# Optimization experiments

Measured on AMD Instinct MI355X. Metric: run time of the kernel, lower is better.

The kernel has to match this reference:

```python
import jax, jax.numpy as jnp
import numpy as np

B, L, D_MODEL, N_HEADS = 2, 2048, 2048, 16
HEAD_DIM = D_MODEL // N_HEADS
EPS = 1e-6
ROPE_THETA = 10000.0


def rms_norm(x, scale):
    # normalize over head_dim, learnable per-dim scale (QKNorm)
    var = jnp.mean(jnp.square(x), axis=-1, keepdims=True)
    return x * jax.lax.rsqrt(var + EPS) * scale


def rope(x, offset=0):
    # x: [B, H, T, D]; rotate-half rotary embedding over flattened positions
    T, D = x.shape[-2], x.shape[-1]
    half = D // 2
    inv_freq = 1.0 / (ROPE_THETA ** (jnp.arange(0, half, dtype=jnp.float32) / half))
    pos = jnp.arange(T, dtype=jnp.float32) + offset
    ang = pos[:, None] * inv_freq[None, :]            # [T, half]
    cos, sin = jnp.cos(ang), jnp.sin(ang)
    x1, x2 = x[..., :half], x[..., half:]
    return jnp.concatenate([x1 * cos - x2 * sin, x1 * sin + x2 * cos], axis=-1)


def setup_inputs() -> dict:
    key = jax.random.key(0)
    ks = jax.random.split(key, 7)
    s = 1.0 / np.sqrt(D_MODEL)
    x = jax.random.normal(ks[0], (B, L, D_MODEL), dtype=jnp.float32)
    w_qkv = jax.random.uniform(ks[1], (D_MODEL, 3 * D_MODEL), jnp.float32, -s, s)
    b_qkv = jax.random.uniform(ks[2], (3 * D_MODEL,), jnp.float32, -s, s)
    q_scale = jnp.ones((HEAD_DIM,), jnp.float32)
    k_scale = jnp.ones((HEAD_DIM,), jnp.float32)
    w_out = jax.random.uniform(ks[3], (D_MODEL, D_MODEL), jnp.float32, -s, s)
    b_out = jax.random.uniform(ks[4], (D_MODEL,), jnp.float32, -s, s)
    mask = jnp.tril(jnp.ones((L, L), dtype=bool))   # causal block mask pattern
    return {"x": x, "w_qkv": w_qkv, "b_qkv": b_qkv, "q_scale": q_scale,
            "k_scale": k_scale, "w_out": w_out, "b_out": b_out, "mask": mask}


def reference(x, w_qkv, b_qkv, q_scale, k_scale, w_out, b_out, mask):
    b, t, _ = x.shape
    qkv = x @ w_qkv + b_qkv                                   # [B, T, 3*D]
    qkv = qkv.reshape(b, t, 3, N_HEADS, HEAD_DIM)
    q, k, v = jnp.moveaxis(qkv, 2, 0)                          # each [B, T, H, D]
    q = jnp.transpose(q, (0, 2, 1, 3))                         # [B, H, T, D]
    k = jnp.transpose(k, (0, 2, 1, 3))
    v = jnp.transpose(v, (0, 2, 1, 3))
    q = rms_norm(q, q_scale)
    k = rms_norm(k, k_scale)
    q = rope(q, offset=0)
    k = rope(k, offset=0)
    scores = jnp.einsum('bhqd,bhkd->bhqk', q, k) / np.sqrt(HEAD_DIM)
    scores = jnp.where(mask[None, None, :, :], scores, jnp.float32(-1e30))
    attn = jax.nn.softmax(scores, axis=-1)
    out = jnp.einsum('bhqk,bhkd->bhqd', attn, v)               # [B, H, T, D]
    out = jnp.transpose(out, (0, 2, 1, 3)).reshape(b, t, D_MODEL)
    return out @ w_out + b_out
```

## Files before the change

kernel.cpp:

```cpp
#include <hip/hip_runtime.h>
#include <hip/hip_bf16.h>
#include <stdint.h>


typedef unsigned short ushort8 __attribute__((ext_vector_type(8)));
typedef short          bf16x8 __attribute__((ext_vector_type(8)));
typedef float          f32x4  __attribute__((ext_vector_type(4)));

#define B_   2
#define L_   2048
#define DM   2048
#define NH   16
#define HD   128
#define QKVW 6144

__device__ __forceinline__ uint16_t f2bf(float f){
  uint32_t u = __builtin_bit_cast(uint32_t, f);
  u += 0x7FFFu + ((u >> 16) & 1u);
  return (uint16_t)(u >> 16);
}
__device__ __forceinline__ float bf2f(uint16_t h){
  uint32_t u = ((uint32_t)h) << 16;
  return __builtin_bit_cast(float, u);
}

#define GLD16(gp, lp) __builtin_amdgcn_global_load_lds( \
  (const __attribute__((address_space(1))) void*)(gp),  \
  (__attribute__((address_space(3))) void*)(lp), 16, 0, 0)

__global__ __launch_bounds__(256) void rope_table(float* __restrict__ ct, float* __restrict__ st){
  int i = blockIdx.x * 256 + threadIdx.x;
  int t = i >> 6, d = i & 63;
  float invf = powf(10000.f, -(float)d * (1.f/64.f));
  float s, c;
  sincosf((float)t * invf, &s, &c);
  ct[i] = c; st[i] = s;
}

__global__ __launch_bounds__(256) void cvt_f32_bf16(const float* __restrict__ x,
                                                    uint16_t* __restrict__ o, int n8){
  int i = blockIdx.x * 256 + threadIdx.x;
  if (i < n8){
    const float4* xv = (const float4*)x;
    float4 a = xv[(size_t)i*2], b = xv[(size_t)i*2+1];
    ushort8 v;
    v[0]=f2bf(a.x); v[1]=f2bf(a.y); v[2]=f2bf(a.z); v[3]=f2bf(a.w);
    v[4]=f2bf(b.x); v[5]=f2bf(b.y); v[6]=f2bf(b.z); v[7]=f2bf(b.w);
    *(ushort8*)(o + (size_t)i*8) = v;
  }
}

__global__ __launch_bounds__(256) void transpose_w(const float* __restrict__ W,
                                                   uint16_t* __restrict__ Wt, int R, int C){
  __shared__ float T[64][65];
  const int rb = blockIdx.x, cb = blockIdx.y;
  const int tid = threadIdx.x;
#pragma unroll
  for (int i=0;i<4;i++){
    int rr = i*16 + (tid >> 4);
    int cc = (tid & 15) * 4;
    float4 v = *(const float4*)(W + (size_t)(rb*64 + rr) * C + cb*64 + cc);
    T[rr][cc] = v.x; T[rr][cc+1] = v.y; T[rr][cc+2] = v.z; T[rr][cc+3] = v.w;
  }
  __syncthreads();
  const int oc = tid >> 2, rc = (tid & 3) * 16;
  ushort8 o0, o1;
#pragma unroll
  for (int j=0;j<8;j++){ o0[j] = f2bf(T[rc+j][oc]); o1[j] = f2bf(T[rc+8+j][oc]); }
  size_t ob = (size_t)(cb*64 + oc) * R + rb*64 + rc;
  *(ushort8*)(Wt + ob)     = o0;
  *(ushort8*)(Wt + ob + 8) = o1;
}

template<int OUTB>
__global__ __launch_bounds__(512, 2) void gemm8p(
    const uint16_t* __restrict__ A, const uint16_t* __restrict__ Bt,
    const float* __restrict__ bias, void* __restrict__ Cv,
    int M, int N, int K, int nbn)
{
  __shared__ uint16_t LA[3*16384];
  __shared__ uint16_t LB[3*8192];
  const int nwg = (M >> 8) * nbn;
  const int q8  = nwg >> 3;
  const int id  = ((int)blockIdx.x & 7) * q8 + ((int)blockIdx.x >> 3);
  const int bm = id / nbn, bn = id % nbn;
  const int tid = threadIdx.x;
  const int lane = tid & 63, w = tid >> 6;
  const int wm = w & 3, wn = w >> 2;
  const int l15 = lane & 15, lh = lane >> 4;
  const int NT = K >> 6;

  const int qs3 = ((lane & 7) ^ ((lane >> 3) & 7)) * 8;
  const uint16_t* gA_ = A  + (size_t)((bm << 8) + (w << 5) + (lane >> 3)) * K + qs3;
  const uint16_t* gB_ = Bt + (size_t)((bn << 7) + (w << 4) + (lane >> 3)) * K + qs3;
  uint16_t* lA_ = LA + (w << 11);
  uint16_t* lB_ = LB + (w << 10);

  const int sw0 = ((lh       ^ (l15 & 7)) << 3);
  const int sw1 = (((4 | lh) ^ (l15 & 7)) << 3);
  const int aoff = (((wm << 6) + l15) << 6);
  const int boff = (((wn << 6) + l15) << 6);

  f32x4 acc[4][4];
#pragma unroll
  for (int i=0;i<4;i++)
#pragma unroll
    for (int j=0;j<4;j++) acc[i][j] = f32x4{0.f,0.f,0.f,0.f};

  auto STAGE_A = [&](int tt, int s, int i){
    GLD16(gA_ + (size_t)tt*64 + (size_t)(i*8)*K, lA_ + s*16384 + i*512);
  };
  auto STAGE_B = [&](int tt, int s, int i){
    GLD16(gB_ + (size_t)tt*64 + (size_t)(i*8)*K, lB_ + s*8192 + i*512);
  };

#pragma unroll
  for (int i=0;i<4;i++) STAGE_A(0, 0, i);
#pragma unroll
  for (int i=0;i<2;i++) STAGE_B(0, 0, i);
#pragma unroll
  for (int i=0;i<4;i++) STAGE_A(1, 1, i);
#pragma unroll
  for (int i=0;i<2;i++) STAGE_B(1, 1, i);
  asm volatile("s_waitcnt vmcnt(6)" ::: "memory");
  __builtin_amdgcn_s_barrier();

  int sl = 0, sl2 = 2;
  for (int t = 0; t < NT; ++t){
    const bool pf = (t + 2 < NT);
    const uint16_t* la = LA + sl*16384;
    const uint16_t* lb = LB + sl*8192;

    bf16x8 af0[4], bf0[4], af1[4], bf1[4];
#pragma unroll
    for (int mi=0;mi<4;mi++) af0[mi] = *(const bf16x8*)(la + aoff + mi*1024 + sw0);
#pragma unroll
    for (int ni=0;ni<4;ni++) bf0[ni] = *(const bf16x8*)(lb + boff + ni*1024 + sw0);
#pragma unroll
    for (int mi=0;mi<4;mi++) af1[mi] = *(const bf16x8*)(la + aoff + mi*1024 + sw1);
#pragma unroll
    for (int ni=0;ni<4;ni++) bf1[ni] = *(const bf16x8*)(lb + boff + ni*1024 + sw1);
    if (pf){
      STAGE_A(t+2, sl2, 0); STAGE_A(t+2, sl2, 1);
      STAGE_A(t+2, sl2, 2); STAGE_A(t+2, sl2, 3);
      STAGE_B(t+2, sl2, 0); STAGE_B(t+2, sl2, 1);
    }
    __builtin_amdgcn_s_setprio(1);
#pragma unroll
    for (int mi=0;mi<4;mi++)
#pragma unroll
      for (int ni=0;ni<4;ni++)
        acc[mi][ni] = __builtin_amdgcn_mfma_f32_16x16x32_bf16(af0[mi], bf0[ni], acc[mi][ni], 0, 0, 0);
#pragma unroll
    for (int mi=0;mi<4;mi++)
#pragma unroll
      for (int ni=0;ni<4;ni++)
        acc[mi][ni] = __builtin_amdgcn_mfma_f32_16x16x32_bf16(af1[mi], bf1[ni], acc[mi][ni], 0, 0, 0);
    __builtin_amdgcn_s_setprio(0);

    if (t < NT-2)       { asm volatile("s_waitcnt vmcnt(6)" ::: "memory"); }
    else if (t == NT-2) { asm volatile("s_waitcnt vmcnt(0)" ::: "memory"); }
    if (t < NT-1) __builtin_amdgcn_s_barrier();
    sl  = (sl  == 2) ? 0 : sl  + 1;
    sl2 = (sl2 == 2) ? 0 : sl2 + 1;
  }

  const int cm = (bm << 8) + (wm << 6);
  const int cn = (bn << 7) + (wn << 6);
#pragma unroll
  for (int ni=0;ni<4;ni++){
    int col = cn + ni*16 + l15;
    float bs = bias[col];
#pragma unroll
    for (int mi=0;mi<4;mi++){
#pragma unroll
      for (int r=0;r<4;r++){
        int rowg = cm + mi*16 + lh*4 + r;
        float v = acc[mi][ni][r] + bs;
        if (OUTB) ((uint16_t*)Cv)[(size_t)rowg * N + col] = f2bf(v);
        else      ((float*)Cv)[(size_t)rowg * N + col] = v;
      }
    }
  }
}

__global__ __launch_bounds__(256) void rmsrope(
    uint16_t* __restrict__ qkv, const float* __restrict__ qs, const float* __restrict__ ks,
    const float* __restrict__ ct, const float* __restrict__ st)
{
  const int bx  = blockIdx.x;
  const int t   = bx & (L_-1);
  const int tid = threadIdx.x;
  const int h   = tid >> 4;
  const int dq  = (tid & 15) * 8;
  const int dd  = dq & 63;
  const bool hi = dq >= 64;
  const size_t base = (size_t)bx * QKVW;
  float cs[8], sn[8];
#pragma unroll
  for (int j=0;j<8;j++){ cs[j] = ct[(size_t)t*64 + dd + j]; sn[j] = st[(size_t)t*64 + dd + j]; }
#pragma unroll
  for (int qk = 0; qk < 2; qk++){
    uint16_t* p = qkv + base + qk*DM + h*HD + dq;
    ushort8 vv = *(const ushort8*)p;
    float x[8]; float ssum = 0.f;
#pragma unroll
    for (int j=0;j<8;j++){ x[j] = bf2f(vv[j]); ssum += x[j]*x[j]; }
    ssum += __shfl_xor(ssum, 1); ssum += __shfl_xor(ssum, 2);
    ssum += __shfl_xor(ssum, 4); ssum += __shfl_xor(ssum, 8);
    const float inv = rsqrtf(ssum * (1.f/128.f) + 1e-6f);
    const float* sc = qk ? ks : qs;
    float y[8];
#pragma unroll
    for (int j=0;j<8;j++) y[j] = x[j] * inv * sc[dq + j];
    float z[8];
#pragma unroll
    for (int j=0;j<8;j++) z[j] = __shfl_xor(y[j], 8);
    ushort8 o;
#pragma unroll
    for (int j=0;j<8;j++){
      float r = hi ? (z[j]*sn[j] + y[j]*cs[j])
                   : (y[j]*cs[j] - z[j]*sn[j]);
      o[j] = f2bf(r);
    }
    *(ushort8*)p = o;
  }
}

__global__ __launch_bounds__(256) void transpose_v(const uint16_t* __restrict__ qkv,
                                                   uint16_t* __restrict__ vt){
  __shared__ uint16_t T[64][136];
  const int tb = blockIdx.x, bh = blockIdx.y;
  const int b = bh >> 4, h = bh & 15;
  const int tid = threadIdx.x;
#pragma unroll
  for (int i=0;i<4;i++){
    int g = i*256 + tid, tt = g >> 4, c = g & 15;
    *(ushort8*)(&T[tt][c*8]) =
      *(const ushort8*)(qkv + ((size_t)b*L_ + tb*64 + tt)*QKVW + 2*DM + h*HD + c*8);
  }
  __syncthreads();
  const int d = tid >> 1, th = tid & 1;
#pragma unroll
  for (int i=0;i<4;i++){
    ushort8 o;
#pragma unroll
    for (int j=0;j<8;j++) o[j] = T[th*32 + i*8 + j][d];
    *(ushort8*)(vt + ((size_t)bh*HD + d)*L_ + tb*64 + th*32 + i*8) = o;
  }
}

__global__ __launch_bounds__(256) void flash_attn(
    const uint16_t* __restrict__ qkv, const uint16_t* __restrict__ vt,
    uint16_t* __restrict__ ao)
{
  const int qp = blockIdx.x;
  const int bh = blockIdx.y;
  const int b = bh >> 4, h = bh & 15;
  const int tid = threadIdx.x;
  const int lane = tid & 63, w = tid >> 6;
  const int l15 = lane & 15, lh = lane >> 4;

  __shared__ uint16_t Ks[64][136];
  __shared__ uint16_t Vs[128][72];
  __shared__ uint16_t Ps[4][16][72];

  const float SCL = 0.12751744f;

  for (int sel = 0; sel < 2; sel++){
    const int qb = sel ? (31 - qp) : qp;

    const size_t qrow = (size_t)b * L_ + qb*64 + w*16 + l15;
    const uint16_t* qp_ = qkv + qrow * QKVW + h * HD;
    bf16x8 qf[4];
#pragma unroll
    for (int c = 0; c < 4; c++) qf[c] = *(const bf16x8*)(qp_ + c*32 + lh*8);

    float m_s = -3.0e38f, l_s = 0.f;
    f32x4 oacc[8];
#pragma unroll
    for (int nt = 0; nt < 8; nt++) oacc[nt] = f32x4{0.f,0.f,0.f,0.f};

    const int ntile = qb + 1;
    ushort8 rk[4], rv[4];

#pragma unroll
    for (int i = 0; i < 4; i++){
      int g = i*256 + tid, row = g >> 4, c = g & 15;
      rk[i] = *(const ushort8*)(qkv + ((size_t)b*L_ + row)*QKVW + DM + h*HD + c*8);
    }
#pragma unroll
    for (int i = 0; i < 4; i++){
      int g = i*256 + tid, d = g >> 3, c = g & 7;
      rv[i] = *(const ushort8*)(vt + ((size_t)bh*HD + d)*L_ + c*8);
    }

    for (int kt = 0; kt < ntile; kt++){
      __syncthreads();
#pragma unroll
      for (int i = 0; i < 4; i++){ int g = i*256+tid; *(ushort8*)(&Ks[g>>4][(g&15)*8]) = rk[i]; }
#pragma unroll
      for (int i = 0; i < 4; i++){ int g = i*256+tid; *(ushort8*)(&Vs[g>>3][(g&7)*8]) = rv[i]; }
      __syncthreads();

      if (kt + 1 < ntile){
        const int k2 = (kt + 1) * 64;
#pragma unroll
        for (int i = 0; i < 4; i++){
          int g = i*256 + tid, row = g >> 4, c = g & 15;
          rk[i] = *(const ushort8*)(qkv + ((size_t)b*L_ + k2 + row)*QKVW + DM + h*HD + c*8);
        }
#pragma unroll
        for (int i = 0; i < 4; i++){
          int g = i*256 + tid, d = g >> 3, c = g & 7;
          rv[i] = *(const ushort8*)(vt + ((size_t)bh*HD + d)*L_ + k2 + c*8);
        }
      }

      f32x4 s[4];
#pragma unroll
      for (int nt = 0; nt < 4; nt++) s[nt] = f32x4{0.f,0.f,0.f,0.f};
      __builtin_amdgcn_s_setprio(1);
#pragma unroll
      for (int c = 0; c < 4; c++){
#pragma unroll
        for (int nt = 0; nt < 4; nt++){
          bf16x8 kf = *(const bf16x8*)(&Ks[nt*16 + l15][c*32 + lh*8]);
          s[nt] = __builtin_amdgcn_mfma_f32_16x16x32_bf16(kf, qf[c], s[nt], 0, 0, 0);
        }
      }
      __builtin_amdgcn_s_setprio(0);

      const bool diag = (kt == qb);
      const int qg = w*16 + l15;
      const int kb = lh*4;
#pragma unroll
      for (int nt = 0; nt < 4; nt++){
#pragma unroll
        for (int r = 0; r < 4; r++){
          float v = s[nt][r] * SCL;
          if (diag && (nt*16 + kb + r > qg)) v = -1.0e30f;
          s[nt][r] = v;
        }
      }
      float pm = s[0][0];
#pragma unroll
      for (int nt = 0; nt < 4; nt++)
#pragma unroll
        for (int r = 0; r < 4; r++) pm = fmaxf(pm, s[nt][r]);
      pm = fmaxf(pm, __shfl_xor(pm, 16));
      pm = fmaxf(pm, __shfl_xor(pm, 32));
      if (!__all(pm - m_s <= 8.0f)){
        float mn = fmaxf(m_s, pm);
        float alpha = exp2f(m_s - mn);
        m_s = mn; l_s *= alpha;
        float ar[4];
#pragma unroll
        for (int r = 0; r < 4; r++) ar[r] = __shfl(alpha, lh*4 + r);
#pragma unroll
        for (int nt = 0; nt < 8; nt++)
#pragma unroll
          for (int r = 0; r < 4; r++) oacc[nt][r] *= ar[r];
      }
      float rs = 0.f;
#pragma unroll
      for (int nt = 0; nt < 4; nt++){
        float p0 = exp2f(s[nt][0] - m_s);
        float p1 = exp2f(s[nt][1] - m_s);
        float p2 = exp2f(s[nt][2] - m_s);
        float p3 = exp2f(s[nt][3] - m_s);
        rs += (p0 + p1) + (p2 + p3);
        uint2 pk;
        pk.x = (uint32_t)f2bf(p0) | ((uint32_t)f2bf(p1) << 16);
        pk.y = (uint32_t)f2bf(p2) | ((uint32_t)f2bf(p3) << 16);
        *(uint2*)(&Ps[w][l15][nt*16 + kb]) = pk;
      }
      rs += __shfl_xor(rs, 16);
      rs += __shfl_xor(rs, 32);
      l_s += rs;

      asm volatile("s_waitcnt lgkmcnt(0)" ::: "memory");
      __builtin_amdgcn_s_setprio(1);
#pragma unroll
      for (int kc = 0; kc < 2; kc++){
        bf16x8 pf = *(const bf16x8*)(&Ps[w][l15][kc*32 + lh*8]);
#pragma unroll
        for (int nt = 0; nt < 8; nt++){
          bf16x8 vf = *(const bf16x8*)(&Vs[nt*16 + l15][kc*32 + lh*8]);
          oacc[nt] = __builtin_amdgcn_mfma_f32_16x16x32_bf16(pf, vf, oacc[nt], 0, 0, 0);
        }
      }
      __builtin_amdgcn_s_setprio(0);
    }
    float invl[4];
#pragma unroll
    for (int r = 0; r < 4; r++) invl[r] = 1.f / __shfl(l_s, lh*4 + r);
#pragma unroll
    for (int nt = 0; nt < 8; nt++){
#pragma unroll
      for (int r = 0; r < 4; r++){
        float v = oacc[nt][r] * invl[r];
        size_t row = (size_t)b*L_ + qb*64 + w*16 + lh*4 + r;
        ao[row * DM + h*HD + nt*16 + l15] = f2bf(v);
      }
    }
  }
}

extern "C" void kernel_launch(void* const* d_in, const int* in_sizes, int n_in,
                              void* d_out, int out_size, void* d_ws, size_t ws_size,
                              hipStream_t stream)
{
  (void)in_sizes; (void)n_in; (void)out_size; (void)ws_size;
  const float* x       = (const float*)d_in[0];
  const float* w_qkv   = (const float*)d_in[1];
  const float* b_qkv   = (const float*)d_in[2];
  const float* q_scale = (const float*)d_in[3];
  const float* k_scale = (const float*)d_in[4];
  const float* w_out   = (const float*)d_in[5];
  const float* b_out   = (const float*)d_in[6];
  float* out = (float*)d_out;

  char* ws = (char*)d_ws;
  uint16_t* qkv   = (uint16_t*)(ws);
  uint16_t* reg1  = (uint16_t*)(ws + 50331648);
  uint16_t* reg2  = (uint16_t*)(ws + 50331648 + 16777216);
  uint16_t* woutT = (uint16_t*)(ws + 50331648 + 16777216 + 25165824);
  float*    ct    = (float*)(ws + 100663296);
  float*    st    = ct + 131072;

  uint16_t* xb    = reg1;
  uint16_t* ao    = reg1;
  uint16_t* wqkvT = reg2;
  uint16_t* vt    = reg2;

  rope_table  <<<512, 256, 0, stream>>>(ct, st);
  cvt_f32_bf16<<<4096, 256, 0, stream>>>(x, xb, 1048576);
  transpose_w <<<dim3(32, 96), 256, 0, stream>>>(w_qkv, wqkvT, 2048, 6144);
  transpose_w <<<dim3(32, 32), 256, 0, stream>>>(w_out, woutT, 2048, 2048);
  gemm8p<1>   <<<768, 512, 0, stream>>>(xb, wqkvT, b_qkv, qkv, 4096, 6144, 2048, 48);
  rmsrope     <<<4096, 256, 0, stream>>>(qkv, q_scale, k_scale, ct, st);
  transpose_v <<<dim3(32, 32), 256, 0, stream>>>(qkv, vt);
  flash_attn  <<<dim3(16, 32), 256, 0, stream>>>(qkv, vt, ao);
  gemm8p<0>   <<<256, 512, 0, stream>>>(ao, woutT, b_out, out, 4096, 2048, 2048, 16);
}
```

Measured before the change: 281.5 us.

## Double query rows per flash-attention block with XOR-swizzled shared memory

Each wave in the flash attention kernel now handles 32 query rows, two 16-row tiles, instead of 16. The query block grows from 64 to 128, so every loaded K/V tile feeds twice as many MFMAs and global K/V traffic is halved. The shared-memory tiles drop their padding and use XOR swizzling to avoid bank conflicts, and the grid is reordered to put batch-head in x. The cost is fewer blocks (256 instead of 512), more registers per thread, and extra masked compute on the two diagonal tiles.

```diff
diff --git a/kernel.cpp b/kernel.cpp
--- a/kernel.cpp
+++ b/kernel.cpp
@@ -254,34 +254,39 @@
     const uint16_t* __restrict__ qkv, const uint16_t* __restrict__ vt,
     uint16_t* __restrict__ ao)
 {
-  const int qp = blockIdx.x;
-  const int bh = blockIdx.y;
+  const int bh = blockIdx.x;
+  const int qp = blockIdx.y;
   const int b = bh >> 4, h = bh & 15;
   const int tid = threadIdx.x;
   const int lane = tid & 63, w = tid >> 6;
   const int l15 = lane & 15, lh = lane >> 4;
-
-  __shared__ uint16_t Ks[64][136];
-  __shared__ uint16_t Vs[128][72];
-  __shared__ uint16_t Ps[4][16][72];
+  const int e3 = l15 & 7;
+
+  __shared__ uint16_t Ks[64][128];
+  __shared__ uint16_t Vs[128][64];
+  __shared__ uint16_t Ps[4][32][64];
 
   const float SCL = 0.12751744f;
 
   for (int sel = 0; sel < 2; sel++){
-    const int qb = sel ? (31 - qp) : qp;
-
-    const size_t qrow = (size_t)b * L_ + qb*64 + w*16 + l15;
-    const uint16_t* qp_ = qkv + qrow * QKVW + h * HD;
-    bf16x8 qf[4];
-#pragma unroll
-    for (int c = 0; c < 4; c++) qf[c] = *(const bf16x8*)(qp_ + c*32 + lh*8);
-
-    float m_s = -3.0e38f, l_s = 0.f;
-    f32x4 oacc[8];
-#pragma unroll
-    for (int nt = 0; nt < 8; nt++) oacc[nt] = f32x4{0.f,0.f,0.f,0.f};
-
-    const int ntile = qb + 1;
+    const int Q = sel ? (15 - qp) : qp;
+
+    const size_t qbase = (size_t)b * L_ + Q*128 + w*32;
+    bf16x8 qf[2][4];
+#pragma unroll
+    for (int qt = 0; qt < 2; qt++)
+#pragma unroll
+      for (int c = 0; c < 4; c++)
+        qf[qt][c] = *(const bf16x8*)(qkv + (qbase + qt*16 + l15)*QKVW + h*HD + c*32 + lh*8);
+
+    float m_s[2] = {-3.0e38f, -3.0e38f}, l_s[2] = {0.f, 0.f};
+    f32x4 oacc[2][8];
+#pragma unroll
+    for (int qt = 0; qt < 2; qt++)
+#pragma unroll
+      for (int nt = 0; nt < 8; nt++) oacc[qt][nt] = f32x4{0.f,0.f,0.f,0.f};
+
+    const int ntile = 2*Q + 2;
     ushort8 rk[4], rv[4];
 
 #pragma unroll
@@ -298,9 +303,15 @@
     for (int kt = 0; kt < ntile; kt++){
       __syncthreads();
 #pragma unroll
-      for (int i = 0; i < 4; i++){ int g = i*256+tid; *(ushort8*)(&Ks[g>>4][(g&15)*8]) = rk[i]; }
-#pragma unroll
-      for (int i = 0; i < 4; i++){ int g = i*256+tid; *(ushort8*)(&Vs[g>>3][(g&7)*8]) = rv[i]; }
+      for (int i = 0; i < 4; i++){
+        int g = i*256 + tid, row = g >> 4, c = g & 15;
+        *(ushort8*)(&Ks[row][(c ^ (row & 7))*8]) = rk[i];
+      }
+#pragma unroll
+      for (int i = 0; i < 4; i++){
+        int g = i*256 + tid, d = g >> 3, c = g & 7;
+        *(ushort8*)(&Vs[d][(c ^ (d & 7))*8]) = rv[i];
+      }
       __syncthreads();
 
       if (kt + 1 < ntile){
@@ -317,91 +328,117 @@
         }
       }
 
-      f32x4 s[4];
-#pragma unroll
-      for (int nt = 0; nt < 4; nt++) s[nt] = f32x4{0.f,0.f,0.f,0.f};
+      f32x4 s[2][4];
+#pragma unroll
+      for (int qt = 0; qt < 2; qt++)
+#pragma unroll
+        for (int nt = 0; nt < 4; nt++) s[qt][nt] = f32x4{0.f,0.f,0.f,0.f};
       __builtin_amdgcn_s_setprio(1);
 #pragma unroll
       for (int c = 0; c < 4; c++){
 #pragma unroll
         for (int nt = 0; nt < 4; nt++){
-          bf16x8 kf = *(const bf16x8*)(&Ks[nt*16 + l15][c*32 + lh*8]);
-          s[nt] = __builtin_amdgcn_mfma_f32_16x16x32_bf16(kf, qf[c], s[nt], 0, 0, 0);
+          bf16x8 kf = *(const bf16x8*)(&Ks[nt*16 + l15][(((c<<2)|lh) ^ e3)*8]);
+          s[0][nt] = __builtin_amdgcn_mfma_f32_16x16x32_bf16(kf, qf[0][c], s[0][nt], 0, 0, 0);
+          s[1][nt] = __builtin_amdgcn_mfma_f32_16x16x32_bf16(kf, qf[1][c], s[1][nt], 0, 0, 0);
         }
       }
       __builtin_amdgcn_s_setprio(0);
 
-      const bool diag = (kt == qb);
-      const int qg = w*16 + l15;
+      const bool edge = (kt >= 2*Q);
       const int kb = lh*4;
-#pragma unroll
-      for (int nt = 0; nt < 4; nt++){
-#pragma unroll
-        for (int r = 0; r < 4; r++){
-          float v = s[nt][r] * SCL;
-          if (diag && (nt*16 + kb + r > qg)) v = -1.0e30f;
-          s[nt][r] = v;
-        }
-      }
-      float pm = s[0][0];
-#pragma unroll
-      for (int nt = 0; nt < 4; nt++)
-#pragma unroll
-        for (int r = 0; r < 4; r++) pm = fmaxf(pm, s[nt][r]);
-      pm = fmaxf(pm, __shfl_xor(pm, 16));
-      pm = fmaxf(pm, __shfl_xor(pm, 32));
-      if (!__all(pm - m_s <= 8.0f)){
-        float mn = fmaxf(m_s, pm);
-        float alpha = exp2f(m_s - mn);
-        m_s = mn; l_s *= alpha;
-        float ar[4];
-#pragma unroll
-        for (int r = 0; r < 4; r++) ar[r] = __shfl(alpha, lh*4 + r);
-#pragma unroll
-        for (int nt = 0; nt < 8; nt++)
-#pragma unroll
-          for (int r = 0; r < 4; r++) oacc[nt][r] *= ar[r];
-      }
-      float rs = 0.f;
-#pragma unroll
-      for (int nt = 0; nt < 4; nt++){
-        float p0 = exp2f(s[nt][0] - m_s);
-        float p1 = exp2f(s[nt][1] - m_s);
-        float p2 = exp2f(s[nt][2] - m_s);
-        float p3 = exp2f(s[nt][3] - m_s);
-        rs += (p0 + p1) + (p2 + p3);
-        uint2 pk;
-        pk.x = (uint32_t)f2bf(p0) | ((uint32_t)f2bf(p1) << 16);
-        pk.y = (uint32_t)f2bf(p2) | ((uint32_t)f2bf(p3) << 16);
-        *(uint2*)(&Ps[w][l15][nt*16 + kb]) = pk;
-      }
-      rs += __shfl_xor(rs, 16);
-      rs += __shfl_xor(rs, 32);
-      l_s += rs;
+      const int q0 = Q*128 + w*32 + l15;
+      const int kglob0 = kt*64 + kb;
+#pragma unroll
+      for (int qt = 0; qt < 2; qt++){
+        const int qg = q0 + qt*16;
+#pragma unroll
+        for (int nt = 0; nt < 4; nt++){
+#pragma unroll
+          for (int r = 0; r < 4; r++){
+            float v = s[qt][nt][r] * SCL;
+            if (edge && (kglob0 + nt*16 + r > qg)) v = -1.0e30f;
+            s[qt][nt][r] = v;
+          }
+        }
+      }
+      float pm[2];
+#pragma unroll
+      for (int qt = 0; qt < 2; qt++){
+        float v = s[qt][0][0];
+#pragma unroll
+        for (int nt = 0; nt < 4; nt++)
+#pragma unroll
+          for (int r = 0; r < 4; r++) v = fmaxf(v, s[qt][nt][r]);
+        v = fmaxf(v, __shfl_xor(v, 16));
+        v = fmaxf(v, __shfl_xor(v, 32));
+        pm[qt] = v;
+      }
+      float grow = fmaxf(pm[0] - m_s[0], pm[1] - m_s[1]);
+      if (!__all(grow <= 8.0f)){
+#pragma unroll
+        for (int qt = 0; qt < 2; qt++){
+          float mn = fmaxf(m_s[qt], pm[qt]);
+          float alpha = exp2f(m_s[qt] - mn);
+          m_s[qt] = mn; l_s[qt] *= alpha;
+          float ar[4];
+#pragma unroll
+          for (int r = 0; r < 4; r++) ar[r] = __shfl(alpha, lh*4 + r);
+#pragma unroll
+          for (int nt = 0; nt < 8; nt++)
+#pragma unroll
+            for (int r = 0; r < 4; r++) oacc[qt][nt][r] *= ar[r];
+        }
+      }
+#pragma unroll
+      for (int qt = 0; qt < 2; qt++){
+        float rs = 0.f;
+#pragma unroll
+        for (int nt = 0; nt < 4; nt++){
+          float p0 = exp2f(s[qt][nt][0] - m_s[qt]);
+          float p1 = exp2f(s[qt][nt][1] - m_s[qt]);
+          float p2 = exp2f(s[qt][nt][2] - m_s[qt]);
+          float p3 = exp2f(s[qt][nt][3] - m_s[qt]);
+          rs += (p0 + p1) + (p2 + p3);
+          uint2 pk;
+          pk.x = (uint32_t)f2bf(p0) | ((uint32_t)f2bf(p1) << 16);
+          pk.y = (uint32_t)f2bf(p2) | ((uint32_t)f2bf(p3) << 16);
+          int ch = ((nt<<1) | (lh>>1)) ^ e3;
+          *(uint2*)(&Ps[w][qt*16 + l15][ch*8 + (lh&1)*4]) = pk;
+        }
+        rs += __shfl_xor(rs, 16);
+        rs += __shfl_xor(rs, 32);
+        l_s[qt] += rs;
+      }
 
       asm volatile("s_waitcnt lgkmcnt(0)" ::: "memory");
       __builtin_amdgcn_s_setprio(1);
 #pragma unroll
       for (int kc = 0; kc < 2; kc++){
-        bf16x8 pf = *(const bf16x8*)(&Ps[w][l15][kc*32 + lh*8]);
+        bf16x8 pf0 = *(const bf16x8*)(&Ps[w][l15]     [(((kc<<2)|lh) ^ e3)*8]);
+        bf16x8 pf1 = *(const bf16x8*)(&Ps[w][16 + l15][(((kc<<2)|lh) ^ e3)*8]);
 #pragma unroll
         for (int nt = 0; nt < 8; nt++){
-          bf16x8 vf = *(const bf16x8*)(&Vs[nt*16 + l15][kc*32 + lh*8]);
-          oacc[nt] = __builtin_amdgcn_mfma_f32_16x16x32_bf16(pf, vf, oacc[nt], 0, 0, 0);
+          bf16x8 vf = *(const bf16x8*)(&Vs[nt*16 + l15][(((kc<<2)|lh) ^ e3)*8]);
+          oacc[0][nt] = __builtin_amdgcn_mfma_f32_16x16x32_bf16(pf0, vf, oacc[0][nt], 0, 0, 0);
+          oacc[1][nt] = __builtin_amdgcn_mfma_f32_16x16x32_bf16(pf1, vf, oacc[1][nt], 0, 0, 0);
         }
       }
       __builtin_amdgcn_s_setprio(0);
     }
-    float invl[4];
-#pragma unroll
-    for (int r = 0; r < 4; r++) invl[r] = 1.f / __shfl(l_s, lh*4 + r);
-#pragma unroll
-    for (int nt = 0; nt < 8; nt++){
-#pragma unroll
-      for (int r = 0; r < 4; r++){
-        float v = oacc[nt][r] * invl[r];
-        size_t row = (size_t)b*L_ + qb*64 + w*16 + lh*4 + r;
-        ao[row * DM + h*HD + nt*16 + l15] = f2bf(v);
+#pragma unroll
+    for (int qt = 0; qt < 2; qt++){
+      float invl[4];
+#pragma unroll
+      for (int r = 0; r < 4; r++) invl[r] = 1.f / __shfl(l_s[qt], lh*4 + r);
+#pragma unroll
+      for (int nt = 0; nt < 8; nt++){
+#pragma unroll
+        for (int r = 0; r < 4; r++){
+          float v = oacc[qt][nt][r] * invl[r];
+          size_t row = qbase + qt*16 + lh*4 + r;
+          ao[row * DM + h*HD + nt*16 + l15] = f2bf(v);
+        }
       }
     }
   }
@@ -441,6 +478,6 @@
   gemm8p<1>   <<<768, 512, 0, stream>>>(xb, wqkvT, b_qkv, qkv, 4096, 6144, 2048, 48);
   rmsrope     <<<4096, 256, 0, stream>>>(qkv, q_scale, k_scale, ct, st);
   transpose_v <<<dim3(32, 32), 256, 0, stream>>>(qkv, vt);
-  flash_attn  <<<dim3(16, 32), 256, 0, stream>>>(qkv, vt, ao);
+  flash_attn  <<<dim3(32, 8), 256, 0, stream>>>(qkv, vt, ao);
   gemm8p<0>   <<<256, 512, 0, stream>>>(ao, woutT, b_out, out, 4096, 2048, 2048, 16);
 }
```

After: 293.0 us. 1.04x slower.

## Fuse QK RMSNorm and RoPE into the QKV GEMM epilogue

Applied to the files above, without the earlier changes.

Removes the separate rmsrope kernel and applies RMSNorm plus rotary embedding in the QKV GEMM epilogue. The B-tile column mapping per wave is changed so that each lane holds both rotate-half partners (d and d+64) of a head. Row sum-of-squares is reduced with lane shuffles and shared memory across the two N-waves. This saves a full read and write pass over Q and K, at the cost of a heavier epilogue with an extra block barrier and scattered 2-byte stores.

```diff
diff --git a/kernel.cpp b/kernel.cpp
--- a/kernel.cpp
+++ b/kernel.cpp
@@ -72,14 +72,17 @@
   *(ushort8*)(Wt + ob + 8) = o1;
 }
 
-template<int OUTB>
+template<int MODE>
 __global__ __launch_bounds__(512, 2) void gemm8p(
     const uint16_t* __restrict__ A, const uint16_t* __restrict__ Bt,
     const float* __restrict__ bias, void* __restrict__ Cv,
-    int M, int N, int K, int nbn)
+    int M, int N, int K, int nbn,
+    const float* __restrict__ qs, const float* __restrict__ ks,
+    const float* __restrict__ ct, const float* __restrict__ st)
 {
   __shared__ uint16_t LA[3*16384];
   __shared__ uint16_t LB[3*8192];
+  __shared__ float sums[4][2][64];
   const int nwg = (M >> 8) * nbn;
   const int q8  = nwg >> 3;
   const int id  = ((int)blockIdx.x & 7) * q8 + ((int)blockIdx.x >> 3);
@@ -99,7 +102,8 @@
   const int sw0 = ((lh       ^ (l15 & 7)) << 3);
   const int sw1 = (((4 | lh) ^ (l15 & 7)) << 3);
   const int aoff = (((wm << 6) + l15) << 6);
-  const int boff = (((wn << 6) + l15) << 6);
+  const int boff = (((wn << 5) + l15) << 6);
+  const int bno[4] = {0, 1024, 4096, 5120};
 
   f32x4 acc[4][4];
 #pragma unroll
@@ -135,11 +139,11 @@
 #pragma unroll
     for (int mi=0;mi<4;mi++) af0[mi] = *(const bf16x8*)(la + aoff + mi*1024 + sw0);
 #pragma unroll
-    for (int ni=0;ni<4;ni++) bf0[ni] = *(const bf16x8*)(lb + boff + ni*1024 + sw0);
+    for (int ni=0;ni<4;ni++) bf0[ni] = *(const bf16x8*)(lb + boff + bno[ni] + sw0);
 #pragma unroll
     for (int mi=0;mi<4;mi++) af1[mi] = *(const bf16x8*)(la + aoff + mi*1024 + sw1);
 #pragma unroll
-    for (int ni=0;ni<4;ni++) bf1[ni] = *(const bf16x8*)(lb + boff + ni*1024 + sw1);
+    for (int ni=0;ni<4;ni++) bf1[ni] = *(const bf16x8*)(lb + boff + bno[ni] + sw1);
     if (pf){
       STAGE_A(t+2, sl2, 0); STAGE_A(t+2, sl2, 1);
       STAGE_A(t+2, sl2, 2); STAGE_A(t+2, sl2, 3);
@@ -166,64 +170,89 @@
   }
 
   const int cm = (bm << 8) + (wm << 6);
-  const int cn = (bn << 7) + (wn << 6);
-#pragma unroll
-  for (int ni=0;ni<4;ni++){
-    int col = cn + ni*16 + l15;
-    float bs = bias[col];
-#pragma unroll
-    for (int mi=0;mi<4;mi++){
+  const int cn = (bn << 7);
+  int dc[4];
+#pragma unroll
+  for (int ni=0;ni<4;ni++) dc[ni] = (wn<<5) + ((ni>>1)<<6) + ((ni&1)<<4) + l15;
+  float bs[4];
+#pragma unroll
+  for (int ni=0;ni<4;ni++) bs[ni] = bias[cn + dc[ni]];
+
+  if (MODE == 0){
+#pragma unroll
+    for (int mi=0;mi<4;mi++)
 #pragma unroll
       for (int r=0;r<4;r++){
         int rowg = cm + mi*16 + lh*4 + r;
-        float v = acc[mi][ni][r] + bs;
-        if (OUTB) ((uint16_t*)Cv)[(size_t)rowg * N + col] = f2bf(v);
-        else      ((float*)Cv)[(size_t)rowg * N + col] = v;
-      }
-    }
-  }
-}
-
-__global__ __launch_bounds__(256) void rmsrope(
-    uint16_t* __restrict__ qkv, const float* __restrict__ qs, const float* __restrict__ ks,
-    const float* __restrict__ ct, const float* __restrict__ st)
-{
-  const int bx  = blockIdx.x;
-  const int t   = bx & (L_-1);
-  const int tid = threadIdx.x;
-  const int h   = tid >> 4;
-  const int dq  = (tid & 15) * 8;
-  const int dd  = dq & 63;
-  const bool hi = dq >= 64;
-  const size_t base = (size_t)bx * QKVW;
-  float cs[8], sn[8];
-#pragma unroll
-  for (int j=0;j<8;j++){ cs[j] = ct[(size_t)t*64 + dd + j]; sn[j] = st[(size_t)t*64 + dd + j]; }
-#pragma unroll
-  for (int qk = 0; qk < 2; qk++){
-    uint16_t* p = qkv + base + qk*DM + h*HD + dq;
-    ushort8 vv = *(const ushort8*)p;
-    float x[8]; float ssum = 0.f;
-#pragma unroll
-    for (int j=0;j<8;j++){ x[j] = bf2f(vv[j]); ssum += x[j]*x[j]; }
-    ssum += __shfl_xor(ssum, 1); ssum += __shfl_xor(ssum, 2);
-    ssum += __shfl_xor(ssum, 4); ssum += __shfl_xor(ssum, 8);
-    const float inv = rsqrtf(ssum * (1.f/128.f) + 1e-6f);
-    const float* sc = qk ? ks : qs;
-    float y[8];
-#pragma unroll
-    for (int j=0;j<8;j++) y[j] = x[j] * inv * sc[dq + j];
-    float z[8];
-#pragma unroll
-    for (int j=0;j<8;j++) z[j] = __shfl_xor(y[j], 8);
-    ushort8 o;
-#pragma unroll
-    for (int j=0;j<8;j++){
-      float r = hi ? (z[j]*sn[j] + y[j]*cs[j])
-                   : (y[j]*cs[j] - z[j]*sn[j]);
-      o[j] = f2bf(r);
-    }
-    *(ushort8*)p = o;
+#pragma unroll
+        for (int ni=0;ni<4;ni++)
+          ((float*)Cv)[(size_t)rowg * N + cn + dc[ni]] = acc[mi][ni][r] + bs[ni];
+      }
+  } else {
+    uint16_t* Cb = (uint16_t*)Cv;
+    const int part = bn >> 4;
+    if (part == 2){
+#pragma unroll
+      for (int mi=0;mi<4;mi++)
+#pragma unroll
+        for (int r=0;r<4;r++){
+          int rowg = cm + mi*16 + lh*4 + r;
+#pragma unroll
+          for (int ni=0;ni<4;ni++)
+            Cb[(size_t)rowg * N + cn + dc[ni]] = f2bf(acc[mi][ni][r] + bs[ni]);
+        }
+    } else {
+      const float* scp = part ? ks : qs;
+      float scv[4];
+#pragma unroll
+      for (int ni=0;ni<4;ni++) scv[ni] = scp[dc[ni]];
+      float ssum[4][4];
+#pragma unroll
+      for (int mi=0;mi<4;mi++)
+#pragma unroll
+        for (int r=0;r<4;r++){
+          float s = 0.f;
+#pragma unroll
+          for (int ni=0;ni<4;ni++){
+            float v = acc[mi][ni][r] + bs[ni];
+            acc[mi][ni][r] = v;
+            s += v*v;
+          }
+          s += __shfl_xor(s, 1); s += __shfl_xor(s, 2);
+          s += __shfl_xor(s, 4); s += __shfl_xor(s, 8);
+          ssum[mi][r] = s;
+        }
+      if (l15 == 0){
+#pragma unroll
+        for (int mi=0;mi<4;mi++)
+#pragma unroll
+          for (int r=0;r<4;r++) sums[wm][wn][mi*16 + lh*4 + r] = ssum[mi][r];
+      }
+      __syncthreads();
+      const int dd0 = (wn<<5) + l15, dd1 = dd0 + 16;
+#pragma unroll
+      for (int mi=0;mi<4;mi++){
+#pragma unroll
+        for (int r=0;r<4;r++){
+          int rid = mi*16 + lh*4 + r;
+          float tot = ssum[mi][r] + sums[wm][wn^1][rid];
+          float iv = rsqrtf(tot * 0.0078125f + 1e-6f);
+          int rowg = cm + rid;
+          int t = rowg & (L_-1);
+          float y0 = acc[mi][0][r] * iv * scv[0];
+          float y1 = acc[mi][1][r] * iv * scv[1];
+          float y2 = acc[mi][2][r] * iv * scv[2];
+          float y3 = acc[mi][3][r] * iv * scv[3];
+          float c0 = ct[t*64 + dd0], s0 = st[t*64 + dd0];
+          float c1 = ct[t*64 + dd1], s1 = st[t*64 + dd1];
+          size_t rb_ = (size_t)rowg * N + cn;
+          Cb[rb_ + dc[0]] = f2bf(y0*c0 - y2*s0);
+          Cb[rb_ + dc[1]] = f2bf(y1*c1 - y3*s1);
+          Cb[rb_ + dc[2]] = f2bf(y0*s0 + y2*c0);
+          Cb[rb_ + dc[3]] = f2bf(y1*s1 + y3*c1);
+        }
+      }
+    }
   }
 }
 
@@ -438,9 +467,10 @@
   cvt_f32_bf16<<<4096, 256, 0, stream>>>(x, xb, 1048576);
   transpose_w <<<dim3(32, 96), 256, 0, stream>>>(w_qkv, wqkvT, 2048, 6144);
   transpose_w <<<dim3(32, 32), 256, 0, stream>>>(w_out, woutT, 2048, 2048);
-  gemm8p<1>   <<<768, 512, 0, stream>>>(xb, wqkvT, b_qkv, qkv, 4096, 6144, 2048, 48);
-  rmsrope     <<<4096, 256, 0, stream>>>(qkv, q_scale, k_scale, ct, st);
+  gemm8p<1>   <<<768, 512, 0, stream>>>(xb, wqkvT, b_qkv, qkv, 4096, 6144, 2048, 48,
+                                        q_scale, k_scale, ct, st);
   transpose_v <<<dim3(32, 32), 256, 0, stream>>>(qkv, vt);
   flash_attn  <<<dim3(16, 32), 256, 0, stream>>>(qkv, vt, ao);
-  gemm8p<0>   <<<256, 512, 0, stream>>>(ao, woutT, b_out, out, 4096, 2048, 2048, 16);
-}
+  gemm8p<0>   <<<256, 512, 0, stream>>>(ao, woutT, b_out, out, 4096, 2048, 2048, 16,
+                                        nullptr, nullptr, nullptr, nullptr);
+}
```

New measurement: 273.2 us. -3.0%, faster.
